# Kernel tuning notes

Hardware: AMD Instinct MI355X
Metric: run time of the kernel (lower is better)

Reference implementation:

```python
import jax, jax.numpy as jnp
import numpy as np

B, LAT, NF, IMG, NC = 16, 512, 32, 128, 12
WT_FIN, WT_FOUT = NF * 64, NF                 # wave_bias_transform dyna 1x1 conv
C2C_FIN, C2C_FH, C2C_FOUT = NF * 4, NF * 2, NF * 2  # cell_to_cell dyna residual block (gated -> fout=2*NF)


def _inorm(x, eps=1e-5):
    # F.instance_norm (no affine): per-sample, per-channel over H,W
    m = x.mean(axis=(2, 3), keepdims=True)
    v = ((x - m) ** 2).mean(axis=(2, 3), keepdims=True)
    return (x - m) * jax.lax.rsqrt(v + eps)


def _sobel_kernels(nf):
    # SinSobel(nf, 3, 1): sin gradient profile x cos smoothing profile, 2 directions (c_factor=2)
    xs = jnp.array([-1.0, 0.0, 1.0], dtype=jnp.float32)
    g = jnp.sin(xs * (np.pi / 2))
    s = jnp.cos(xs * (np.pi / 2))
    ky = jnp.outer(g, s)
    kx = jnp.outer(s, g)
    k = jnp.stack([ky, kx])[:, None]          # [2,1,3,3]
    return jnp.tile(k, (nf, 1, 1, 1))         # [2*nf,1,3,3] depthwise


def _hyper(lat, w1, b1, w2, b2):
    h = jax.nn.relu(lat @ w1 + b1)
    return h @ w2 + b2


def _dyn_params(p, fin, fout, off):
    w = p[:, off:off + fin * fout].reshape(-1, fout, fin) / np.sqrt(fin)
    b = p[:, off + fin * fout: off + fin * fout + fout]
    return w, b, off + fin * fout + fout


def _econv(x, w, b):
    # per-sample dynamic 1x1 conv: x [B,I,H,W], w [B,O,I], b [B,O]
    return jnp.einsum('bihw,boi->bohw', x, w) + b[:, :, None, None]


def setup_inputs():
    key = jax.random.key(0)
    ks = jax.random.split(key, 8)
    sc = 0.02
    P = (C2C_FIN * C2C_FH + C2C_FH) + (C2C_FH * C2C_FH + C2C_FH) + \
        (C2C_FH * C2C_FOUT + C2C_FOUT) + (C2C_FIN * C2C_FOUT + C2C_FOUT)
    WP = WT_FIN * WT_FOUT + WT_FOUT
    return {
        'lat': jax.random.normal(ks[0], (B, LAT), jnp.float32),
        'leak_factor': jnp.asarray(0.1, jnp.float32),
        'wave_bias': jax.random.normal(ks[1], (1, WT_FIN, IMG, IMG), jnp.float32),
        'wt_w1': jax.random.normal(ks[2], (LAT, LAT), jnp.float32) * sc,
        'wt_b1': jnp.zeros((LAT,), jnp.float32),
        'wt_w2': jax.random.normal(ks[3], (LAT, WP), jnp.float32) * sc,
        'wt_b2': jnp.zeros((WP,), jnp.float32),
        'c2c_w1': jax.random.normal(ks[4], (LAT, 2 * LAT), jnp.float32) * sc,
        'c2c_b1': jnp.zeros((2 * LAT,), jnp.float32),
        'c2c_w2': jax.random.normal(ks[5], (2 * LAT, P), jnp.float32) * sc,
        'c2c_b2': jnp.zeros((P,), jnp.float32),
        'out_w': jax.random.normal(ks[6], (3, NF), jnp.float32) / np.sqrt(NF),
        'out_b': jnp.zeros((3,), jnp.float32),
    }


def reference(lat, leak_factor, wave_bias, wt_w1, wt_b1, wt_w2, wt_b2,
              c2c_w1, c2c_b1, c2c_w2, c2c_b2, out_w, out_b):
    b = lat.shape[0]
    # wave bias: per-sample dynamic 1x1 conv -> exp(i*x) -> cat(real, imag) -> instance norm
    pw = _hyper(lat, wt_w1, wt_b1, wt_w2, wt_b2)
    ww, wbb, _ = _dyn_params(pw, WT_FIN, WT_FOUT, 0)
    wb_flat = _econv(jnp.broadcast_to(wave_bias, (b,) + wave_bias.shape[1:]), ww, wbb)
    wave = _inorm(jnp.concatenate([jnp.cos(wb_flat), jnp.sin(wb_flat)], axis=1))  # [B,2*NF,H,W]
    leak = jnp.clip(leak_factor, 1e-3, 1e3)
    # cell_to_cell hypernetwork-generated residual-block weights (shared across calls)
    p = _hyper(lat, c2c_w1, c2c_b1, c2c_w2, c2c_b2)
    w_in, b_in, o = _dyn_params(p, C2C_FIN, C2C_FH, 0)
    w_mid, b_mid, o = _dyn_params(p, C2C_FH, C2C_FH, o)
    w_out, b_out, o = _dyn_params(p, C2C_FH, C2C_FOUT, o)
    w_sk, b_sk, o = _dyn_params(p, C2C_FIN, C2C_FOUT, o)
    kern = _sobel_kernels(NF)

    def step(out, _):
        g = _inorm(jax.lax.conv_general_dilated(
            out, kern, (1, 1), 'SAME', feature_group_count=NF,
            dimension_numbers=('NCHW', 'OIHW', 'NCHW')))
        xin = jnp.concatenate([g, wave], axis=1)             # [B,4*NF,H,W]
        h = jax.nn.leaky_relu(_econv(xin, w_in, b_in), 0.2)
        h = jax.nn.leaky_relu(_econv(h, w_mid, b_mid), 0.2)
        y = _econv(h, w_out, b_out) + _econv(xin, w_sk, b_sk)  # [B,2*NF,H,W]
        out_new = y[:, :NF] * jax.nn.sigmoid(y[:, NF:])        # gated
        nxt = out + leak * out_new
        return nxt, nxt

    out0 = jnp.zeros((b, NF, IMG, IMG), jnp.float32)
    out, embs = jax.lax.scan(step, out0, None, length=NC)
    out_embs = jnp.concatenate([out0[None], embs], axis=0)     # [NC+1,B,NF,H,W]
    out_raw = jnp.einsum('bihw,oi->bohw', out, out_w) + out_b[None, :, None, None]
    return jnp.clip(out_raw, -1.0, 1.0), out_embs, out_raw
```

## Files before the change

kernel.cpp:

```cpp
#include <hip/hip_runtime.h>
#include <hip/hip_bf16.h>
#include <stdint.h>


typedef __attribute__((ext_vector_type(8))) short s8v;
typedef __attribute__((ext_vector_type(4))) float f4v;

__device__ __forceinline__ uint16_t f2b(float f) {
    uint32_t x = __builtin_bit_cast(uint32_t, f);
    uint32_t r = (x + 0x7fffu + ((x >> 16) & 1u)) >> 16;
    return (uint16_t)r;
}

__device__ __forceinline__ float blockReduceSum(float v, float* scratch) {
    #pragma unroll
    for (int o = 32; o > 0; o >>= 1) v += __shfl_down(v, o, 64);
    int w = threadIdx.x >> 6;
    if ((threadIdx.x & 63) == 0) scratch[w] = v;
    __syncthreads();
    float r = scratch[0] + scratch[1] + scratch[2] + scratch[3];
    __syncthreads();
    return r;
}

__global__ __launch_bounds__(256) void k_hyper1(const float* __restrict__ lat,
        const float* __restrict__ w1a, const float* __restrict__ b1a,
        const float* __restrict__ w1b, const float* __restrict__ b1b,
        float* __restrict__ hwtT, float* __restrict__ hc2cT) {
    int b = blockIdx.y;
    int j = blockIdx.x * 256 + threadIdx.x;
    __shared__ float lats[512];
    for (int k = threadIdx.x; k < 512; k += 256) lats[k] = lat[b * 512 + k];
    __syncthreads();
    if (j < 512) {
        float acc = b1a[j];
        #pragma unroll 4
        for (int k = 0; k < 512; k++) acc += lats[k] * w1a[k * 512 + j];
        hwtT[j * 16 + b] = fmaxf(acc, 0.f);
    } else {
        int jj = j - 512;
        float acc = b1b[jj];
        #pragma unroll 4
        for (int k = 0; k < 512; k++) acc += lats[k] * w1b[k * 1024 + jj];
        hc2cT[jj * 16 + b] = fmaxf(acc, 0.f);
    }
}

__global__ __launch_bounds__(256) void k_hyper2(const float* __restrict__ hT,
        const float* __restrict__ w2, const float* __restrict__ b2v,
        float* __restrict__ outp, int K, int N) {
    extern __shared__ float hs[];
    for (int i = threadIdx.x; i < K * 16; i += 256) hs[i] = hT[i];
    __syncthreads();
    int col = blockIdx.x * 256 + threadIdx.x;
    if (col >= N) return;
    float acc[16];
    float bias = b2v[col];
    #pragma unroll
    for (int b = 0; b < 16; b++) acc[b] = bias;
    #pragma unroll 4
    for (int k = 0; k < K; k++) {
        float wv = w2[(size_t)k * N + col];
        const f4v* h4 = (const f4v*)(hs + k * 16);
        f4v h0 = h4[0], h1 = h4[1], h2 = h4[2], h3 = h4[3];
        acc[0]  += h0[0] * wv; acc[1]  += h0[1] * wv; acc[2]  += h0[2] * wv; acc[3]  += h0[3] * wv;
        acc[4]  += h1[0] * wv; acc[5]  += h1[1] * wv; acc[6]  += h1[2] * wv; acc[7]  += h1[3] * wv;
        acc[8]  += h2[0] * wv; acc[9]  += h2[1] * wv; acc[10] += h2[2] * wv; acc[11] += h2[3] * wv;
        acc[12] += h3[0] * wv; acc[13] += h3[1] * wv; acc[14] += h3[2] * wv; acc[15] += h3[3] * wv;
    }
    #pragma unroll
    for (int b = 0; b < 16; b++) outp[(size_t)b * N + col] = acc[b];
}

__global__ __launch_bounds__(256) void k_prepw(const float* __restrict__ pw, const float* __restrict__ pc,
        uint16_t* __restrict__ ww, uint16_t* __restrict__ wc) {
    int tid = blockIdx.x * 256 + threadIdx.x;
    const float s128 = 0.08838834764831845f;
    const float s64  = 0.125f;
    const float s2048 = 0.02209708691207961f;
    if (tid < 16 * 65536) {
        int b = tid >> 16, r = tid & 65535;
        ww[tid] = f2b(pw[(size_t)b * 65568 + r] * s2048);
    } else {
        int t = tid - 16 * 65536;
        int b = t / 24576, r = t % 24576;
        int src; float sc;
        if (r < 8192)       { src = r;                   sc = s128; }
        else if (r < 12288) { src = 8256  + (r - 8192);  sc = s64; }
        else if (r < 16384) { src = 12416 + (r - 12288); sc = s64; }
        else                { src = 16576 + (r - 16384); sc = s128; }
        wc[(size_t)b * 24576 + r] = f2b(pc[(size_t)b * 24832 + src] * sc);
    }
}

__global__ __launch_bounds__(256) void k_transpose(const float* __restrict__ wb, uint16_t* __restrict__ wbt) {
    __shared__ uint16_t tile[64][66];
    int p0 = blockIdx.x * 64, i0 = blockIdx.y * 64;
    int lane = threadIdx.x & 63, grp = threadIdx.x >> 6;
    #pragma unroll
    for (int r = 0; r < 16; r++) {
        int i = grp * 16 + r;
        tile[i][lane] = f2b(wb[(size_t)(i0 + i) * 16384 + p0 + lane]);
    }
    __syncthreads();
    #pragma unroll
    for (int r = 0; r < 16; r++) {
        int p = grp * 16 + r;
        wbt[(size_t)(p0 + p) * 2048 + i0 + lane] = tile[lane][p];
    }
}

__global__ __launch_bounds__(256) void k_wavegemm(const uint16_t* __restrict__ ww,
        const uint16_t* __restrict__ wbt, const float* __restrict__ pw, float* __restrict__ wb) {
    int id = blockIdx.x;
    int xcd = id & 7, slot = id >> 3;
    int nt = xcd * 8 + (slot >> 3);
    int mt = slot & 7;
    int w = threadIdx.x >> 6, L = threadIdx.x & 63;
    int l15 = L & 15, quad = L >> 4;
    int pxbase = nt * 256 + w * 64;
    f4v acc[4][4];
    #pragma unroll
    for (int t = 0; t < 4; t++) {
        int m = mt * 64 + t * 16 + quad * 4;
        int b = m >> 5, o = m & 31;
        f4v bv = *(const f4v*)(pw + (size_t)b * 65568 + 65536 + o);
        #pragma unroll
        for (int j = 0; j < 4; j++) acc[t][j] = bv;
    }
    #pragma unroll 2
    for (int kk = 0; kk < 64; kk++) {
        s8v a[4], x[4];
        #pragma unroll
        for (int t = 0; t < 4; t++) {
            int m = mt * 64 + t * 16 + l15;
            a[t] = *(const s8v*)(ww + (size_t)m * 2048 + kk * 32 + quad * 8);
        }
        #pragma unroll
        for (int j = 0; j < 4; j++) {
            int p = pxbase + j * 16 + l15;
            x[j] = *(const s8v*)(wbt + (size_t)p * 2048 + kk * 32 + quad * 8);
        }
        #pragma unroll
        for (int t = 0; t < 4; t++)
            #pragma unroll
            for (int j = 0; j < 4; j++)
                acc[t][j] = __builtin_amdgcn_mfma_f32_16x16x32_bf16(a[t], x[j], acc[t][j], 0, 0, 0);
    }
    #pragma unroll
    for (int t = 0; t < 4; t++)
        #pragma unroll
        for (int j = 0; j < 4; j++)
            #pragma unroll
            for (int r = 0; r < 4; r++) {
                int row = mt * 64 + t * 16 + quad * 4 + r;
                int p = pxbase + j * 16 + l15;
                wb[(size_t)row * 16384 + p] = acc[t][j][r];
            }
}

__global__ __launch_bounds__(256) void k_wavestats(const float* __restrict__ wb, float* __restrict__ stats) {
    __shared__ float scratch[4];
    int c = blockIdx.x, b = blockIdx.y;
    const float* src = wb + (size_t)(b * 32 + c) * 16384;
    float sc = 0.f, sc2 = 0.f, ss = 0.f, ss2 = 0.f;
    for (int p = threadIdx.x; p < 16384; p += 256) {
        float x = src[p];
        float cv = __cosf(x), sv = __sinf(x);
        sc += cv; sc2 += cv * cv; ss += sv; ss2 += sv * sv;
    }
    float SC  = blockReduceSum(sc,  scratch);
    float SC2 = blockReduceSum(sc2, scratch);
    float SS  = blockReduceSum(ss,  scratch);
    float SS2 = blockReduceSum(ss2, scratch);
    if (threadIdx.x == 0) {
        float mc = SC * (1.f / 16384.f);
        float vc = fmaxf(SC2 * (1.f / 16384.f) - mc * mc, 0.f);
        float ms = SS * (1.f / 16384.f);
        float vs = fmaxf(SS2 * (1.f / 16384.f) - ms * ms, 0.f);
        stats[(b * 64 + c) * 2 + 0] = mc;
        stats[(b * 64 + c) * 2 + 1] = rsqrtf(vc + 1e-5f);
        stats[(b * 64 + 32 + c) * 2 + 0] = ms;
        stats[(b * 64 + 32 + c) * 2 + 1] = rsqrtf(vs + 1e-5f);
    }
}

__global__ __launch_bounds__(256) void k_wavewrite(const float* __restrict__ wb,
        const float* __restrict__ stats, uint16_t* __restrict__ xin) {
    __shared__ uint16_t tl[256][66];
    __shared__ float sst[128];
    int b = blockIdx.y, p0 = blockIdx.x * 256;
    int t = threadIdx.x;
    if (t < 128) sst[t] = stats[b * 128 + t];
    __syncthreads();
    for (int c = 0; c < 32; c++) {
        int row = b * 32 + c;
        float x = wb[(size_t)row * 16384 + p0 + t];
        float cv = __cosf(x), sv = __sinf(x);
        tl[t][c]      = f2b((cv - sst[2 * c]) * sst[2 * c + 1]);
        tl[t][c + 32] = f2b((sv - sst[64 + 2 * c]) * sst[64 + 2 * c + 1]);
    }
    __syncthreads();
    uint16_t* dst = xin + ((size_t)(b * 16384 + p0 + t) * 128 + 64);
    const uint32_t* s32 = (const uint32_t*)&tl[t][0];
    #pragma unroll
    for (int c8 = 0; c8 < 64; c8 += 8) {
        uint4 v;
        v.x = s32[c8 / 2 + 0]; v.y = s32[c8 / 2 + 1];
        v.z = s32[c8 / 2 + 2]; v.w = s32[c8 / 2 + 3];
        *(uint4*)(dst + c8) = v;
    }
}

__global__ __launch_bounds__(256) void k_gstats(const float* __restrict__ prev, float* __restrict__ stats) {
    __shared__ float scratch[4];
    int ic = blockIdx.x, b = blockIdx.y;
    const float* src = prev + (size_t)(b * 32 + ic) * 16384;
    float sy = 0.f, sy2 = 0.f, sx = 0.f, sx2 = 0.f;
    for (int p = threadIdx.x; p < 16384; p += 256) {
        int y = p >> 7, x = p & 127;
        float up = (y > 0)   ? src[p - 128] : 0.f;
        float dn = (y < 127) ? src[p + 128] : 0.f;
        float lf = (x > 0)   ? src[p - 1]   : 0.f;
        float rt = (x < 127) ? src[p + 1]   : 0.f;
        float vy = dn - up, vx = rt - lf;
        sy += vy; sy2 += vy * vy; sx += vx; sx2 += vx * vx;
    }
    float SY  = blockReduceSum(sy,  scratch);
    float SY2 = blockReduceSum(sy2, scratch);
    float SX  = blockReduceSum(sx,  scratch);
    float SX2 = blockReduceSum(sx2, scratch);
    if (threadIdx.x == 0) {
        float my = SY * (1.f / 16384.f);
        float vy = fmaxf(SY2 * (1.f / 16384.f) - my * my, 0.f);
        float mx = SX * (1.f / 16384.f);
        float vx = fmaxf(SX2 * (1.f / 16384.f) - mx * mx, 0.f);
        stats[(b * 64 + 2 * ic) * 2 + 0] = my;
        stats[(b * 64 + 2 * ic) * 2 + 1] = rsqrtf(vy + 1e-5f);
        stats[(b * 64 + 2 * ic + 1) * 2 + 0] = mx;
        stats[(b * 64 + 2 * ic + 1) * 2 + 1] = rsqrtf(vx + 1e-5f);
    }
}

__global__ __launch_bounds__(256) void k_gwrite(const float* __restrict__ prev,
        const float* __restrict__ stats, uint16_t* __restrict__ xin) {
    __shared__ uint16_t tl[256][66];
    int b = blockIdx.y, p0 = blockIdx.x * 256;
    int t = threadIdx.x;
    int p = p0 + t;
    int y = p >> 7, x = p & 127;
    for (int ic = 0; ic < 32; ic++) {
        const float* src = prev + (size_t)(b * 32 + ic) * 16384;
        float up = (y > 0)   ? src[p - 128] : 0.f;
        float dn = (y < 127) ? src[p + 128] : 0.f;
        float lf = (x > 0)   ? src[p - 1]   : 0.f;
        float rt = (x < 127) ? src[p + 1]   : 0.f;
        int o = 2 * ic;
        float m0 = stats[(b * 64 + o) * 2], r0 = stats[(b * 64 + o) * 2 + 1];
        float m1 = stats[(b * 64 + o + 1) * 2], r1 = stats[(b * 64 + o + 1) * 2 + 1];
        tl[t][o]     = f2b((dn - up - m0) * r0);
        tl[t][o + 1] = f2b((rt - lf - m1) * r1);
    }
    __syncthreads();
    uint16_t* dst = xin + (size_t)(b * 16384 + p) * 128;
    const uint32_t* s32 = (const uint32_t*)&tl[t][0];
    #pragma unroll
    for (int c8 = 0; c8 < 64; c8 += 8) {
        uint4 v;
        v.x = s32[c8 / 2 + 0]; v.y = s32[c8 / 2 + 1];
        v.z = s32[c8 / 2 + 2]; v.w = s32[c8 / 2 + 3];
        *(uint4*)(dst + c8) = v;
    }
}

__global__ __launch_bounds__(256) void k_conv(const uint16_t* __restrict__ wc,
        const uint16_t* __restrict__ xin, const float* __restrict__ pc,
        const float* __restrict__ prev, float* __restrict__ next,
        const float* __restrict__ leakp) {
    __shared__ uint16_t Hs[256][72];
    int b = blockIdx.y, p0 = blockIdx.x * 256;
    int w = threadIdx.x >> 6, L = threadIdx.x & 63;
    int l15 = L & 15, quad = L >> 4;
    const uint16_t* wcb = wc + (size_t)b * 24576;
    const float* pcb = pc + (size_t)b * 24832;
    size_t xbase = ((size_t)b * 16384 + p0 + w * 64) * 128;

    f4v acc1[4][4], acc3[4][4];
    #pragma unroll
    for (int t = 0; t < 4; t++) {
        f4v bv1 = *(const f4v*)(pcb + 8192 + t * 16 + quad * 4);
        f4v bo  = *(const f4v*)(pcb + 16512 + t * 16 + quad * 4);
        f4v bs  = *(const f4v*)(pcb + 24768 + t * 16 + quad * 4);
        f4v bv3 = bo + bs;
        #pragma unroll
        for (int j = 0; j < 4; j++) { acc1[t][j] = bv1; acc3[t][j] = bv3; }
    }
    #pragma unroll
    for (int kk = 0; kk < 4; kk++) {
        s8v x[4];
        #pragma unroll
        for (int j = 0; j < 4; j++)
            x[j] = *(const s8v*)(xin + xbase + (size_t)(j * 16 + l15) * 128 + kk * 32 + quad * 8);
        #pragma unroll
        for (int t = 0; t < 4; t++) {
            s8v a1 = *(const s8v*)(wcb + (size_t)(t * 16 + l15) * 128 + kk * 32 + quad * 8);
            #pragma unroll
            for (int j = 0; j < 4; j++)
                acc1[t][j] = __builtin_amdgcn_mfma_f32_16x16x32_bf16(a1, x[j], acc1[t][j], 0, 0, 0);
        }
        #pragma unroll
        for (int t = 0; t < 4; t++) {
            s8v a3 = *(const s8v*)(wcb + 16384 + (size_t)(t * 16 + l15) * 128 + kk * 32 + quad * 8);
            #pragma unroll
            for (int j = 0; j < 4; j++)
                acc3[t][j] = __builtin_amdgcn_mfma_f32_16x16x32_bf16(a3, x[j], acc3[t][j], 0, 0, 0);
        }
    }
    #pragma unroll
    for (int t = 0; t < 4; t++)
        #pragma unroll
        for (int j = 0; j < 4; j++) {
            uint16_t pk[4];
            #pragma unroll
            for (int r = 0; r < 4; r++) {
                float v = acc1[t][j][r];
                pk[r] = f2b(v > 0.f ? v : 0.2f * v);
            }
            int px = w * 64 + j * 16 + l15;
            int ch = t * 16 + quad * 4;
            uint2 u; u.x = (uint32_t)pk[0] | ((uint32_t)pk[1] << 16);
            u.y = (uint32_t)pk[2] | ((uint32_t)pk[3] << 16);
            *(uint2*)&Hs[px][ch] = u;
        }
    __syncthreads();

    f4v acc2[4][4];
    #pragma unroll
    for (int t = 0; t < 4; t++) {
        f4v bv = *(const f4v*)(pcb + 12352 + t * 16 + quad * 4);
        #pragma unroll
        for (int j = 0; j < 4; j++) acc2[t][j] = bv;
    }
    #pragma unroll
    for (int kk = 0; kk < 2; kk++) {
        s8v a[4], h[4];
        #pragma unroll
        for (int t = 0; t < 4; t++)
            a[t] = *(const s8v*)(wcb + 8192 + (size_t)(t * 16 + l15) * 64 + kk * 32 + quad * 8);
        #pragma unroll
        for (int j = 0; j < 4; j++) {
            int px = w * 64 + j * 16 + l15;
            h[j] = *(const s8v*)&Hs[px][kk * 32 + quad * 8];
        }
        #pragma unroll
        for (int t = 0; t < 4; t++)
            #pragma unroll
            for (int j = 0; j < 4; j++)
                acc2[t][j] = __builtin_amdgcn_mfma_f32_16x16x32_bf16(a[t], h[j], acc2[t][j], 0, 0, 0);
    }
    __syncthreads();
    #pragma unroll
    for (int t = 0; t < 4; t++)
        #pragma unroll
        for (int j = 0; j < 4; j++) {
            uint16_t pk[4];
            #pragma unroll
            for (int r = 0; r < 4; r++) {
                float v = acc2[t][j][r];
                pk[r] = f2b(v > 0.f ? v : 0.2f * v);
            }
            int px = w * 64 + j * 16 + l15;
            int ch = t * 16 + quad * 4;
            uint2 u; u.x = (uint32_t)pk[0] | ((uint32_t)pk[1] << 16);
            u.y = (uint32_t)pk[2] | ((uint32_t)pk[3] << 16);
            *(uint2*)&Hs[px][ch] = u;
        }
    __syncthreads();

    #pragma unroll
    for (int kk = 0; kk < 2; kk++) {
        s8v a[4], h[4];
        #pragma unroll
        for (int t = 0; t < 4; t++)
            a[t] = *(const s8v*)(wcb + 12288 + (size_t)(t * 16 + l15) * 64 + kk * 32 + quad * 8);
        #pragma unroll
        for (int j = 0; j < 4; j++) {
            int px = w * 64 + j * 16 + l15;
            h[j] = *(const s8v*)&Hs[px][kk * 32 + quad * 8];
        }
        #pragma unroll
        for (int t = 0; t < 4; t++)
            #pragma unroll
            for (int j = 0; j < 4; j++)
                acc3[t][j] = __builtin_amdgcn_mfma_f32_16x16x32_bf16(a[t], h[j], acc3[t][j], 0, 0, 0);
    }

    float leak = leakp[0];
    leak = fminf(fmaxf(leak, 0.001f), 1000.f);
    #pragma unroll
    for (int t = 0; t < 2; t++)
        #pragma unroll
        for (int j = 0; j < 4; j++) {
            int px = p0 + w * 64 + j * 16 + l15;
            #pragma unroll
            for (int r = 0; r < 4; r++) {
                int ch = t * 16 + quad * 4 + r;
                float y1 = acc3[t][j][r];
                float y2 = acc3[t + 2][j][r];
                float on = y1 / (1.f + __expf(-y2));
                size_t idx = (size_t)(b * 32 + ch) * 16384 + px;
                next[idx] = prev[idx] + leak * on;
            }
        }
}

__global__ __launch_bounds__(256) void k_final(const float* __restrict__ outs,
        const float* __restrict__ ow, const float* __restrict__ ob,
        float* __restrict__ dclip, float* __restrict__ draw) {
    __shared__ float ws[3][32];
    __shared__ float obs[3];
    int b = blockIdx.y, p0 = blockIdx.x * 256;
    int t = threadIdx.x;
    if (t < 96) ws[t / 32][t % 32] = ow[t];
    if (t < 3) obs[t] = ob[t];
    __syncthreads();
    int p = p0 + t;
    float a0 = obs[0], a1 = obs[1], a2 = obs[2];
    #pragma unroll 4
    for (int c = 0; c < 32; c++) {
        float v = outs[(size_t)(b * 32 + c) * 16384 + p];
        a0 += v * ws[0][c]; a1 += v * ws[1][c]; a2 += v * ws[2][c];
    }
    float raw[3] = {a0, a1, a2};
    #pragma unroll
    for (int oc = 0; oc < 3; oc++) {
        size_t idx = (size_t)(b * 3 + oc) * 16384 + p;
        draw[idx] = raw[oc];
        dclip[idx] = fminf(fmaxf(raw[oc], -1.f), 1.f);
    }
}

extern "C" void kernel_launch(void* const* d_in, const int* in_sizes, int n_in,
                              void* d_out, int out_size, void* d_ws, size_t ws_size,
                              hipStream_t stream) {
    const float* lat   = (const float*)d_in[0];
    const float* leakp = (const float*)d_in[1];
    const float* wbias = (const float*)d_in[2];
    const float* wtw1  = (const float*)d_in[3];
    const float* wtb1  = (const float*)d_in[4];
    const float* wtw2  = (const float*)d_in[5];
    const float* wtb2  = (const float*)d_in[6];
    const float* cw1   = (const float*)d_in[7];
    const float* cb1   = (const float*)d_in[8];
    const float* cw2   = (const float*)d_in[9];
    const float* cb2   = (const float*)d_in[10];
    const float* outw  = (const float*)d_in[11];
    const float* outb  = (const float*)d_in[12];
    float* out_f = (float*)d_out;

    char* ws = (char*)d_ws;
    float*    hwtT  = (float*)(ws + 0);
    float*    hc2cT = (float*)(ws + 32768);
    float*    pw    = (float*)(ws + 98304);
    float*    pc    = (float*)(ws + 4294656);
    uint16_t* ww    = (uint16_t*)(ws + 5883904);
    uint16_t* wc    = (uint16_t*)(ws + 7981056);
    float*    statw = (float*)(ws + 8767488);
    float*    statg = (float*)(ws + 8775680);
    float*    wb    = (float*)(ws + 8783872);
    uint16_t* wbt   = (uint16_t*)(ws + 42338304);
    uint16_t* xin   = (uint16_t*)(ws + 109447168);

    float* emb0 = out_f + 786432;

    hipMemsetAsync(emb0, 0, 33554432, stream);
    hipMemsetAsync(statg, 0, 8192, stream);

    k_hyper1<<<dim3(6, 16), 256, 0, stream>>>(lat, wtw1, wtb1, cw1, cb1, hwtT, hc2cT);
    k_hyper2<<<dim3(257), 256, 32768, stream>>>(hwtT, wtw2, wtb2, pw, 512, 65568);
    k_hyper2<<<dim3(97), 256, 65536, stream>>>(hc2cT, cw2, cb2, pc, 1024, 24832);
    k_prepw<<<dim3(5632), 256, 0, stream>>>(pw, pc, ww, wc);
    k_transpose<<<dim3(256, 32), 256, 0, stream>>>(wbias, wbt);
    k_wavegemm<<<dim3(512), 256, 0, stream>>>(ww, wbt, pw, wb);
    k_wavestats<<<dim3(32, 16), 256, 0, stream>>>(wb, statw);
    k_wavewrite<<<dim3(64, 16), 256, 0, stream>>>(wb, statw, xin);

    for (int it = 0; it < 12; ++it) {
        const float* prev = emb0 + (size_t)it * 8388608;
        float* next = emb0 + (size_t)(it + 1) * 8388608;
        if (it > 0)
            k_gstats<<<dim3(32, 16), 256, 0, stream>>>(prev, statg);
        k_gwrite<<<dim3(64, 16), 256, 0, stream>>>(prev, statg, xin);
        k_conv<<<dim3(64, 16), 256, 0, stream>>>(wc, xin, pc, prev, next, leakp);
    }
    k_final<<<dim3(64, 16), 256, 0, stream>>>(emb0 + (size_t)12 * 8388608, outw, outb,
                                              out_f, out_f + 109838336);
}
```

Before: 2.331 ms.

## Fuse sobel-gradient normalization into conv kernel via shared memory

The per-step k_gwrite kernel is removed. k_conv now computes the normalized sobel gradient channels for its 256-pixel tile directly into a shared-memory buffer and feeds them to the MFMA input stage from LDS. The wave channels are stored in a compact 64-channel buffer instead of the upper half of a 128-channel interleaved buffer. This drops one launch and a full bf16 write and read of the gradient half of xin per step. In exchange, k_conv takes on the stencil loads and a shared buffer that is reused across stages, which adds extra barriers.

```diff
diff --git a/kernel.cpp b/kernel.cpp
--- a/kernel.cpp
+++ b/kernel.cpp
@@ -186,7 +186,7 @@
 }
 
 __global__ __launch_bounds__(256) void k_wavewrite(const float* __restrict__ wb,
-        const float* __restrict__ stats, uint16_t* __restrict__ xin) {
+        const float* __restrict__ stats, uint16_t* __restrict__ xinw) {
     __shared__ uint16_t tl[256][66];
     __shared__ float sst[128];
     int b = blockIdx.y, p0 = blockIdx.x * 256;
@@ -201,7 +201,7 @@
         tl[t][c + 32] = f2b((sv - sst[64 + 2 * c]) * sst[64 + 2 * c + 1]);
     }
     __syncthreads();
-    uint16_t* dst = xin + ((size_t)(b * 16384 + p0 + t) * 128 + 64);
+    uint16_t* dst = xinw + (size_t)(b * 16384 + p0 + t) * 64;
     const uint32_t* s32 = (const uint32_t*)&tl[t][0];
     #pragma unroll
     for (int c8 = 0; c8 < 64; c8 += 8) {
@@ -242,138 +242,137 @@
     }
 }
 
-__global__ __launch_bounds__(256) void k_gwrite(const float* __restrict__ prev,
-        const float* __restrict__ stats, uint16_t* __restrict__ xin) {
-    __shared__ uint16_t tl[256][66];
+__global__ __launch_bounds__(256) void k_conv(const uint16_t* __restrict__ wc,
+        const uint16_t* __restrict__ xinw, const float* __restrict__ pc,
+        const float* __restrict__ statg,
+        const float* __restrict__ prev, float* __restrict__ next,
+        const float* __restrict__ leakp) {
+    __shared__ uint16_t XH[256][72];
     int b = blockIdx.y, p0 = blockIdx.x * 256;
     int t = threadIdx.x;
-    int p = p0 + t;
-    int y = p >> 7, x = p & 127;
-    for (int ic = 0; ic < 32; ic++) {
-        const float* src = prev + (size_t)(b * 32 + ic) * 16384;
-        float up = (y > 0)   ? src[p - 128] : 0.f;
-        float dn = (y < 127) ? src[p + 128] : 0.f;
-        float lf = (x > 0)   ? src[p - 1]   : 0.f;
-        float rt = (x < 127) ? src[p + 1]   : 0.f;
-        int o = 2 * ic;
-        float m0 = stats[(b * 64 + o) * 2], r0 = stats[(b * 64 + o) * 2 + 1];
-        float m1 = stats[(b * 64 + o + 1) * 2], r1 = stats[(b * 64 + o + 1) * 2 + 1];
-        tl[t][o]     = f2b((dn - up - m0) * r0);
-        tl[t][o + 1] = f2b((rt - lf - m1) * r1);
-    }
-    __syncthreads();
-    uint16_t* dst = xin + (size_t)(b * 16384 + p) * 128;
-    const uint32_t* s32 = (const uint32_t*)&tl[t][0];
-    #pragma unroll
-    for (int c8 = 0; c8 < 64; c8 += 8) {
-        uint4 v;
-        v.x = s32[c8 / 2 + 0]; v.y = s32[c8 / 2 + 1];
-        v.z = s32[c8 / 2 + 2]; v.w = s32[c8 / 2 + 3];
-        *(uint4*)(dst + c8) = v;
-    }
-}
-
-__global__ __launch_bounds__(256) void k_conv(const uint16_t* __restrict__ wc,
-        const uint16_t* __restrict__ xin, const float* __restrict__ pc,
-        const float* __restrict__ prev, float* __restrict__ next,
-        const float* __restrict__ leakp) {
-    __shared__ uint16_t Hs[256][72];
-    int b = blockIdx.y, p0 = blockIdx.x * 256;
-    int w = threadIdx.x >> 6, L = threadIdx.x & 63;
+    int w = t >> 6, L = t & 63;
     int l15 = L & 15, quad = L >> 4;
     const uint16_t* wcb = wc + (size_t)b * 24576;
     const float* pcb = pc + (size_t)b * 24832;
-    size_t xbase = ((size_t)b * 16384 + p0 + w * 64) * 128;
+
+    {
+        int p = p0 + t;
+        int y = p >> 7, x = p & 127;
+        for (int ic = 0; ic < 32; ic++) {
+            const float* src = prev + (size_t)(b * 32 + ic) * 16384;
+            float up = (y > 0)   ? src[p - 128] : 0.f;
+            float dn = (y < 127) ? src[p + 128] : 0.f;
+            float lf = (x > 0)   ? src[p - 1]   : 0.f;
+            float rt = (x < 127) ? src[p + 1]   : 0.f;
+            int o = 2 * ic;
+            float m0 = statg[(b * 64 + o) * 2],     r0 = statg[(b * 64 + o) * 2 + 1];
+            float m1 = statg[(b * 64 + o + 1) * 2], r1 = statg[(b * 64 + o + 1) * 2 + 1];
+            uint32_t u = (uint32_t)f2b((dn - up - m0) * r0)
+                       | ((uint32_t)f2b((rt - lf - m1) * r1) << 16);
+            *(uint32_t*)&XH[t][o] = u;
+        }
+    }
+    __syncthreads();
+
+    size_t xwbase = ((size_t)b * 16384 + p0 + w * 64) * 64;
 
     f4v acc1[4][4], acc3[4][4];
     #pragma unroll
-    for (int t = 0; t < 4; t++) {
-        f4v bv1 = *(const f4v*)(pcb + 8192 + t * 16 + quad * 4);
-        f4v bo  = *(const f4v*)(pcb + 16512 + t * 16 + quad * 4);
-        f4v bs  = *(const f4v*)(pcb + 24768 + t * 16 + quad * 4);
+    for (int tt = 0; tt < 4; tt++) {
+        f4v bv1 = *(const f4v*)(pcb + 8192 + tt * 16 + quad * 4);
+        f4v bo  = *(const f4v*)(pcb + 16512 + tt * 16 + quad * 4);
+        f4v bs  = *(const f4v*)(pcb + 24768 + tt * 16 + quad * 4);
         f4v bv3 = bo + bs;
         #pragma unroll
-        for (int j = 0; j < 4; j++) { acc1[t][j] = bv1; acc3[t][j] = bv3; }
+        for (int j = 0; j < 4; j++) { acc1[tt][j] = bv1; acc3[tt][j] = bv3; }
     }
     #pragma unroll
     for (int kk = 0; kk < 4; kk++) {
         s8v x[4];
         #pragma unroll
-        for (int j = 0; j < 4; j++)
-            x[j] = *(const s8v*)(xin + xbase + (size_t)(j * 16 + l15) * 128 + kk * 32 + quad * 8);
-        #pragma unroll
-        for (int t = 0; t < 4; t++) {
-            s8v a1 = *(const s8v*)(wcb + (size_t)(t * 16 + l15) * 128 + kk * 32 + quad * 8);
+        for (int j = 0; j < 4; j++) {
+            int px = w * 64 + j * 16 + l15;
+            if (kk < 2)
+                x[j] = *(const s8v*)&XH[px][kk * 32 + quad * 8];
+            else
+                x[j] = *(const s8v*)(xinw + xwbase + (size_t)(j * 16 + l15) * 64
+                                     + (kk - 2) * 32 + quad * 8);
+        }
+        #pragma unroll
+        for (int tt = 0; tt < 4; tt++) {
+            s8v a1 = *(const s8v*)(wcb + (size_t)(tt * 16 + l15) * 128 + kk * 32 + quad * 8);
             #pragma unroll
             for (int j = 0; j < 4; j++)
-                acc1[t][j] = __builtin_amdgcn_mfma_f32_16x16x32_bf16(a1, x[j], acc1[t][j], 0, 0, 0);
-        }
-        #pragma unroll
-        for (int t = 0; t < 4; t++) {
-            s8v a3 = *(const s8v*)(wcb + 16384 + (size_t)(t * 16 + l15) * 128 + kk * 32 + quad * 8);
+                acc1[tt][j] = __builtin_amdgcn_mfma_f32_16x16x32_bf16(a1, x[j], acc1[tt][j], 0, 0, 0);
+        }
+        #pragma unroll
+        for (int tt = 0; tt < 4; tt++) {
+            s8v a3 = *(const s8v*)(wcb + 16384 + (size_t)(tt * 16 + l15) * 128 + kk * 32 + quad * 8);
             #pragma unroll
             for (int j = 0; j < 4; j++)
-                acc3[t][j] = __builtin_amdgcn_mfma_f32_16x16x32_bf16(a3, x[j], acc3[t][j], 0, 0, 0);
-        }
-    }
-    #pragma unroll
-    for (int t = 0; t < 4; t++)
+                acc3[tt][j] = __builtin_amdgcn_mfma_f32_16x16x32_bf16(a3, x[j], acc3[tt][j], 0, 0, 0);
+        }
+    }
+    __syncthreads();
+
+    #pragma unroll
+    for (int tt = 0; tt < 4; tt++)
         #pragma unroll
         for (int j = 0; j < 4; j++) {
             uint16_t pk[4];
             #pragma unroll
             for (int r = 0; r < 4; r++) {
-                float v = acc1[t][j][r];
+                float v = acc1[tt][j][r];
                 pk[r] = f2b(v > 0.f ? v : 0.2f * v);
             }
             int px = w * 64 + j * 16 + l15;
-            int ch = t * 16 + quad * 4;
+            int ch = tt * 16 + quad * 4;
             uint2 u; u.x = (uint32_t)pk[0] | ((uint32_t)pk[1] << 16);
             u.y = (uint32_t)pk[2] | ((uint32_t)pk[3] << 16);
-            *(uint2*)&Hs[px][ch] = u;
+            *(uint2*)&XH[px][ch] = u;
         }
     __syncthreads();
 
     f4v acc2[4][4];
     #pragma unroll
-    for (int t = 0; t < 4; t++) {
-        f4v bv = *(const f4v*)(pcb + 12352 + t * 16 + quad * 4);
-        #pragma unroll
-        for (int j = 0; j < 4; j++) acc2[t][j] = bv;
+    for (int tt = 0; tt < 4; tt++) {
+        f4v bv = *(const f4v*)(pcb + 12352 + tt * 16 + quad * 4);
+        #pragma unroll
+        for (int j = 0; j < 4; j++) acc2[tt][j] = bv;
     }
     #pragma unroll
     for (int kk = 0; kk < 2; kk++) {
         s8v a[4], h[4];
         #pragma unroll
-        for (int t = 0; t < 4; t++)
-            a[t] = *(const s8v*)(wcb + 8192 + (size_t)(t * 16 + l15) * 64 + kk * 32 + quad * 8);
+        for (int tt = 0; tt < 4; tt++)
+            a[tt] = *(const s8v*)(wcb + 8192 + (size_t)(tt * 16 + l15) * 64 + kk * 32 + quad * 8);
         #pragma unroll
         for (int j = 0; j < 4; j++) {
             int px = w * 64 + j * 16 + l15;
-            h[j] = *(const s8v*)&Hs[px][kk * 32 + quad * 8];
-        }
-        #pragma unroll
-        for (int t = 0; t < 4; t++)
+            h[j] = *(const s8v*)&XH[px][kk * 32 + quad * 8];
+        }
+        #pragma unroll
+        for (int tt = 0; tt < 4; tt++)
             #pragma unroll
             for (int j = 0; j < 4; j++)
-                acc2[t][j] = __builtin_amdgcn_mfma_f32_16x16x32_bf16(a[t], h[j], acc2[t][j], 0, 0, 0);
-    }
-    __syncthreads();
-    #pragma unroll
-    for (int t = 0; t < 4; t++)
+                acc2[tt][j] = __builtin_amdgcn_mfma_f32_16x16x32_bf16(a[tt], h[j], acc2[tt][j], 0, 0, 0);
+    }
+    __syncthreads();
+    #pragma unroll
+    for (int tt = 0; tt < 4; tt++)
         #pragma unroll
         for (int j = 0; j < 4; j++) {
             uint16_t pk[4];
             #pragma unroll
             for (int r = 0; r < 4; r++) {
-                float v = acc2[t][j][r];
+                float v = acc2[tt][j][r];
                 pk[r] = f2b(v > 0.f ? v : 0.2f * v);
             }
             int px = w * 64 + j * 16 + l15;
-            int ch = t * 16 + quad * 4;
+            int ch = tt * 16 + quad * 4;
             uint2 u; u.x = (uint32_t)pk[0] | ((uint32_t)pk[1] << 16);
             u.y = (uint32_t)pk[2] | ((uint32_t)pk[3] << 16);
-            *(uint2*)&Hs[px][ch] = u;
+            *(uint2*)&XH[px][ch] = u;
         }
     __syncthreads();
 
@@ -381,32 +380,32 @@
     for (int kk = 0; kk < 2; kk++) {
         s8v a[4], h[4];
         #pragma unroll
-        for (int t = 0; t < 4; t++)
-            a[t] = *(const s8v*)(wcb + 12288 + (size_t)(t * 16 + l15) * 64 + kk * 32 + quad * 8);
+        for (int tt = 0; tt < 4; tt++)
+            a[tt] = *(const s8v*)(wcb + 12288 + (size_t)(tt * 16 + l15) * 64 + kk * 32 + quad * 8);
         #pragma unroll
         for (int j = 0; j < 4; j++) {
             int px = w * 64 + j * 16 + l15;
-            h[j] = *(const s8v*)&Hs[px][kk * 32 + quad * 8];
-        }
-        #pragma unroll
-        for (int t = 0; t < 4; t++)
+            h[j] = *(const s8v*)&XH[px][kk * 32 + quad * 8];
+        }
+        #pragma unroll
+        for (int tt = 0; tt < 4; tt++)
             #pragma unroll
             for (int j = 0; j < 4; j++)
-                acc3[t][j] = __builtin_amdgcn_mfma_f32_16x16x32_bf16(a[t], h[j], acc3[t][j], 0, 0, 0);
+                acc3[tt][j] = __builtin_amdgcn_mfma_f32_16x16x32_bf16(a[tt], h[j], acc3[tt][j], 0, 0, 0);
     }
 
     float leak = leakp[0];
     leak = fminf(fmaxf(leak, 0.001f), 1000.f);
     #pragma unroll
-    for (int t = 0; t < 2; t++)
+    for (int tt = 0; tt < 2; tt++)
         #pragma unroll
         for (int j = 0; j < 4; j++) {
             int px = p0 + w * 64 + j * 16 + l15;
             #pragma unroll
             for (int r = 0; r < 4; r++) {
-                int ch = t * 16 + quad * 4 + r;
-                float y1 = acc3[t][j][r];
-                float y2 = acc3[t + 2][j][r];
+                int ch = tt * 16 + quad * 4 + r;
+                float y1 = acc3[tt][j][r];
+                float y2 = acc3[tt + 2][j][r];
                 float on = y1 / (1.f + __expf(-y2));
                 size_t idx = (size_t)(b * 32 + ch) * 16384 + px;
                 next[idx] = prev[idx] + leak * on;
@@ -469,7 +468,7 @@
     float*    statg = (float*)(ws + 8775680);
     float*    wb    = (float*)(ws + 8783872);
     uint16_t* wbt   = (uint16_t*)(ws + 42338304);
-    uint16_t* xin   = (uint16_t*)(ws + 109447168);
+    uint16_t* xinw  = (uint16_t*)(ws + 109447168);
 
     float* emb0 = out_f + 786432;
 
@@ -483,15 +482,14 @@
     k_transpose<<<dim3(256, 32), 256, 0, stream>>>(wbias, wbt);
     k_wavegemm<<<dim3(512), 256, 0, stream>>>(ww, wbt, pw, wb);
     k_wavestats<<<dim3(32, 16), 256, 0, stream>>>(wb, statw);
-    k_wavewrite<<<dim3(64, 16), 256, 0, stream>>>(wb, statw, xin);
+    k_wavewrite<<<dim3(64, 16), 256, 0, stream>>>(wb, statw, xinw);
 
     for (int it = 0; it < 12; ++it) {
         const float* prev = emb0 + (size_t)it * 8388608;
         float* next = emb0 + (size_t)(it + 1) * 8388608;
         if (it > 0)
             k_gstats<<<dim3(32, 16), 256, 0, stream>>>(prev, statg);
-        k_gwrite<<<dim3(64, 16), 256, 0, stream>>>(prev, statg, xin);
-        k_conv<<<dim3(64, 16), 256, 0, stream>>>(wc, xin, pc, prev, next, leakp);
+        k_conv<<<dim3(64, 16), 256, 0, stream>>>(wc, xinw, pc, statg, prev, next, leakp);
     }
     k_final<<<dim3(64, 16), 256, 0, stream>>>(emb0 + (size_t)12 * 8388608, outw, outb,
                                               out_f, out_f + 109838336);
```

New measurement: 2.484 ms. 1.07x slower.
